# Kernel tuning notes

Measured on AMD Instinct MI355X. Metric: run time of the kernel, lower is better.

The kernel has to match this reference:

```python
import jax, jax.numpy as jnp
import numpy as np

B, N, D, H, CD = 2, 2048, 1024, 16, 3
HD = D // H


def setup_inputs() -> dict:
    key = jax.random.key(0)
    ks = jax.random.split(key, 6)
    x = jax.random.normal(ks[0], (B, N, D), dtype=jnp.float32)
    coords = jax.random.normal(ks[1], (B, N, CD), dtype=jnp.float32)
    attn_bias = jax.random.normal(ks[2], (N, N), dtype=jnp.float32) * 0.1
    Wqkv = jax.random.normal(ks[3], (D, 3 * D), dtype=jnp.float32) * (1.0 / np.sqrt(D))
    bqkv = jnp.zeros((3 * D,), dtype=jnp.float32)
    rel_weight = jax.random.normal(ks[4], (H, CD), dtype=jnp.float32) * 0.02
    return {"x": x, "coords": coords, "attn_bias": attn_bias, "Wqkv": Wqkv,
            "bqkv": bqkv, "rel_weight": rel_weight}


def reference(x, coords, attn_bias, Wqkv, bqkv, rel_weight):
    b, n, d = x.shape
    h, hd = H, HD
    qkv = x @ Wqkv + bqkv                       # (B,N,3D)
    q, k, v = jnp.split(qkv, 3, axis=-1)
    # reshape_for_mha: (B,N,D) -> (B,H,N,hd)
    def heads(t):
        return t.reshape(b, n, h, hd).transpose(0, 2, 1, 3)
    qh, kh, vh = heads(q), heads(k), heads(v)
    # coord_proj[b,h,n] = coords[b,n,:] @ rel_weight[h,:]
    coord_proj = jnp.einsum('bnc,hc->bhn', coords.astype(jnp.float32), rel_weight)
    # flex_attention: scale by 1/sqrt(head_dim) BEFORE score_mod
    scores = jnp.einsum('bhqd,bhkd->bhqk', qh, kh) / np.sqrt(hd)
    scores = scores + coord_proj[:, :, :, None] - coord_proj[:, :, None, :]
    scores = scores + attn_bias[None, None, :, :]   # '2d' additive mask bias
    attn = jax.nn.softmax(scores, axis=-1)
    yh = jnp.einsum('bhqk,bhkd->bhqd', attn, vh)    # (B,H,N,hd)
    return yh.transpose(0, 2, 1, 3).reshape(b, n, d)
```

## Files before the change

### kernel.cpp

```cpp
#include <hip/hip_runtime.h>
#include <hip/hip_bf16.h>
#include <math.h>

typedef __hip_bfloat16 bf16;
typedef __bf16  bf16x8 __attribute__((ext_vector_type(8)));
typedef float   f32x4  __attribute__((ext_vector_type(4)));

#define BB 2
#define NN 2048
#define DD 1024
#define HH 16
#define HD 64
#define LOG2E   1.44269504f
#define SCALE_Q 0.18033688f

__device__ __forceinline__ void glds16(const bf16* g, bf16* l) {
    __builtin_amdgcn_global_load_lds((const __attribute__((address_space(1))) void*)g,
                                     (__attribute__((address_space(3))) void*)l, 16, 0, 0);
}
__device__ __forceinline__ unsigned short bfu(float x) {
    bf16 b = __float2bfloat16(x);
    return __builtin_bit_cast(unsigned short, b);
}

__global__ __launch_bounds__(256) void prep(const float* __restrict__ x,
                                            const float* __restrict__ bias,
                                            const float* __restrict__ W,
                                            const float* __restrict__ coords,
                                            const float* __restrict__ relw,
                                            bf16* __restrict__ xb,
                                            unsigned* __restrict__ pbh,
                                            bf16* __restrict__ Wt,
                                            bf16* __restrict__ cpn) {
    __shared__ bf16 tsm[64][65];
    const int bid = blockIdx.x, tid = threadIdx.x;
    if (bid < 2048) {
        size_t i = ((size_t)bid * 256 + tid) * 8;
        float4 a = *(const float4*)(x + i);
        float4 b = *(const float4*)(x + i + 4);
        bf16 t[8];
        t[0] = __float2bfloat16(a.x); t[1] = __float2bfloat16(a.y);
        t[2] = __float2bfloat16(a.z); t[3] = __float2bfloat16(a.w);
        t[4] = __float2bfloat16(b.x); t[5] = __float2bfloat16(b.y);
        t[6] = __float2bfloat16(b.z); t[7] = __float2bfloat16(b.w);
        *(int4*)(xb + i) = *(int4*)t;
    } else if (bid < 3072) {
        int tt   = (bid - 2048) * 256 + tid;
        int lane = tt & 63;
        int wave = (tt >> 6) & 7;
        int kt   = (tt >> 9) & 31;
        int Qb   = tt >> 14;
        int quad = lane >> 4, l15 = lane & 15;
        unsigned pk[8];
#pragma unroll
        for (int m = 0; m < 8; ++m) {
            int g = m >> 1, rp = m & 1;
            int q = Qb * 128 + wave * 16 + quad * 4 + rp * 2;
            int k = kt * 64 + g * 16 + l15;
            float v0 = LOG2E * bias[(size_t)q * NN + k];
            float v1 = LOG2E * bias[(size_t)(q + 1) * NN + k];
            pk[m] = (unsigned)bfu(v0) | ((unsigned)bfu(v1) << 16);
        }
        int4* dst = (int4*)(pbh + (size_t)tt * 8);
        dst[0] = ((int4*)pk)[0];
        dst[1] = ((int4*)pk)[1];
    } else if (bid < 3840) {
        int idx = bid - 3072;
        int n0 = (idx % 48) * 64;
        int k0 = (idx / 48) * 64;
        int tx = tid & 63, tg = tid >> 6;
#pragma unroll
        for (int i = 0; i < 16; ++i) {
            int r = tg + i * 4;
            tsm[r][tx] = __float2bfloat16(W[(size_t)(k0 + r) * 3072 + n0 + tx]);
        }
        __syncthreads();
#pragma unroll
        for (int i = 0; i < 16; ++i) {
            int r = tg + i * 4;
            Wt[(size_t)(n0 + r) * 1024 + k0 + tx] = tsm[tx][r];
        }
    } else {
        int idx = (bid - 3840) * 256 + tid;
        int n  = idx & (NN - 1);
        int bh = idx >> 11;
        int h  = bh & (HH - 1);
        int b  = bh >> 4;
        float acc = 0.f;
#pragma unroll
        for (int c = 0; c < 3; ++c)
            acc += coords[(size_t)(b * NN + n) * 3 + c] * relw[h * 3 + c];
        cpn[idx] = __float2bfloat16(-LOG2E * acc);
    }
}

__global__ __launch_bounds__(256) void qkv_gemm(const bf16* __restrict__ X,
                                                const bf16* __restrict__ W,
                                                const float* __restrict__ bq,
                                                bf16* __restrict__ qo,
                                                bf16* __restrict__ ko,
                                                bf16* __restrict__ vt) {
    __shared__ __align__(16) bf16 As[128 * 32];
    __shared__ __align__(16) bf16 Bs[128 * 32];
    const int tid  = threadIdx.x;
    const int gid  = blockIdx.x + blockIdx.y * 24;
    const int xcd  = gid & 7;
    const int idx  = gid >> 3;
    const int n0   = (idx >> 2) * 128;
    const int m0   = (xcd * 4 + (idx & 3)) * 128;
    const int wave = tid >> 6, lane = tid & 63, l15 = lane & 15, quad = lane >> 4;
    const int wm   = wave >> 1, wn = wave & 1;

    f32x4 acc[4][4];
    const f32x4 z4 = {0.f, 0.f, 0.f, 0.f};
#pragma unroll
    for (int i = 0; i < 4; ++i)
#pragma unroll
        for (int j = 0; j < 4; ++j) acc[i][j] = z4;

    for (int kt = 0; kt < 1024; kt += 32) {
        __syncthreads();
#pragma unroll
        for (int j = 0; j < 2; ++j) {
            int s   = (wave * 2 + j) * 64 + lane;
            int row = s >> 2;
            int c   = (s & 3) ^ ((row >> 1) & 3);
            glds16(X + (size_t)(m0 + row) * 1024 + kt + c * 8, As + (wave * 2 + j) * 512);
            glds16(W + (size_t)(n0 + row) * 1024 + kt + c * 8, Bs + (wave * 2 + j) * 512);
        }
        __syncthreads();

        bf16x8 a[4], b[4];
#pragma unroll
        for (int mt = 0; mt < 4; ++mt) {
            int ra = wm * 64 + mt * 16 + l15;
            a[mt] = *(const bf16x8*)&As[ra * 32 + ((quad ^ ((ra >> 1) & 3)) * 8)];
        }
#pragma unroll
        for (int nt = 0; nt < 4; ++nt) {
            int rb = wn * 64 + nt * 16 + l15;
            b[nt] = *(const bf16x8*)&Bs[rb * 32 + ((quad ^ ((rb >> 1) & 3)) * 8)];
        }
#pragma unroll
        for (int mt = 0; mt < 4; ++mt)
#pragma unroll
            for (int nt = 0; nt < 4; ++nt)
                acc[mt][nt] = __builtin_amdgcn_mfma_f32_16x16x32_bf16(a[mt], b[nt], acc[mt][nt], 0, 0, 0);
    }

#pragma unroll
    for (int nt = 0; nt < 4; ++nt) {
        int c    = n0 + wn * 64 + nt * 16 + l15;
        int tsel = c >> 10;
        int rem  = c & 1023;
        int h    = rem >> 6, d = rem & 63;
        float bias = bq[c];
        float qs   = (tsel == 0) ? SCALE_Q : 1.0f;
#pragma unroll
        for (int mt = 0; mt < 4; ++mt)
#pragma unroll
            for (int r = 0; r < 4; ++r) {
                int m = m0 + wm * 64 + mt * 16 + quad * 4 + r;
                int b = m >> 11, n = m & (NN - 1);
                bf16 val = __float2bfloat16((acc[mt][nt][r] + bias) * qs);
                if (tsel == 2)
                    vt[((size_t)(b * HH + h) * HD + d) * NN + n] = val;
                else
                    ((tsel == 1) ? ko : qo)[((size_t)(b * HH + h) * NN + n) * HD + d] = val;
            }
    }
}

__global__ __launch_bounds__(512, 4) void attn(const bf16* __restrict__ Q,
                                               const bf16* __restrict__ K,
                                               const bf16* __restrict__ Vt_g,
                                               const bf16* __restrict__ cpn_g,
                                               const unsigned* __restrict__ pbh,
                                               float* __restrict__ out) {
    __shared__ __align__(16) bf16 Ks[2][64 * 64];
    __shared__ __align__(16) bf16 Vs[2][64 * 64];
    __shared__ __align__(16) unsigned PsW[8][16 * 36];
    __shared__ __align__(16) bf16 cpl[NN];
    const int tid  = threadIdx.x;
    const int Qb   = blockIdx.x;
    const int bh   = blockIdx.y;
    const int b    = bh >> 4, h = bh & 15;
    const int q0   = Qb * 128;
    const int wave = tid >> 6, lane = tid & 63, l15 = lane & 15, quad = lane >> 4;
    const size_t base = (size_t)bh * NN * HD;

    if (wave < 4)
        glds16(cpn_g + bh * NN + (wave * 64 + lane) * 8, cpl + wave * 512);

    const int qrow = q0 + wave * 16 + l15;
    bf16x8 qf0 = *(const bf16x8*)&Q[base + (size_t)qrow * HD + quad * 8];
    bf16x8 qf1 = *(const bf16x8*)&Q[base + (size_t)qrow * HD + 32 + quad * 8];

    const int ps   = wave * 64 + lane;
    const int prow = ps >> 3;
    const int pcol = (ps & 7) ^ (prow & 7);

    glds16(K    + base + (size_t)prow * HD + pcol * 8, Ks[0] + wave * 512);
    glds16(Vt_g + base + (size_t)prow * NN + pcol * 8, Vs[0] + wave * 512);

    const unsigned* bptr = pbh + ((((size_t)Qb * 32) * 8 + wave) * 64 + lane) * 8;
    unsigned bvA[8], bvB[8];
    *(int4*)&bvA[0] = ((const int4*)bptr)[0];
    *(int4*)&bvA[4] = ((const int4*)bptr)[1];

    const f32x4 z4 = {0.f, 0.f, 0.f, 0.f};
    f32x4 l4 = z4;
    f32x4 o[4];
#pragma unroll
    for (int t = 0; t < 4; ++t) o[t] = z4;

#define ATTN_TILE(T, CUR, BVC, BVN)                                               \
    {                                                                             \
        __syncthreads();     \
        if ((T) < 31) {                   \
            int kk1 = ((T) + 1) * 64;                                             \
            glds16(K    + base + (size_t)(kk1 + prow) * HD + pcol * 8,            \
                   Ks[(CUR) ^ 1] + wave * 512);                                   \
            glds16(Vt_g + base + (size_t)prow * NN + kk1 + pcol * 8,              \
                   Vs[(CUR) ^ 1] + wave * 512);                                   \
            const unsigned* bp = bptr + (size_t)((T) + 1) * 4096;                 \
            *(int4*)&BVN[0] = ((const int4*)bp)[0];                               \
            *(int4*)&BVN[4] = ((const int4*)bp)[1];                               \
        }                                                                         \
               \
        f32x4 p4[4];                                                              \
        _Pragma("unroll")                                                         \
        for (int g = 0; g < 4; ++g) {                                             \
            float mgv = __bfloat162float(cpl[(T) * 64 + g * 16 + l15]);           \
            unsigned ba = BVC[g * 2], bb2 = BVC[g * 2 + 1];                       \
            f32x4 c0;                                                             \
            c0[0] = __builtin_bit_cast(float, ba << 16) + mgv;                    \
            c0[1] = __builtin_bit_cast(float, ba & 0xffff0000u) + mgv;            \
            c0[2] = __builtin_bit_cast(float, bb2 << 16) + mgv;                   \
            c0[3] = __builtin_bit_cast(float, bb2 & 0xffff0000u) + mgv;           \
            int krow = g * 16 + l15, sw = krow & 7;                               \
            bf16x8 k0 = *(const bf16x8*)&Ks[(CUR)][krow * 64 + ((quad ^ sw) * 8)];         \
            bf16x8 k1 = *(const bf16x8*)&Ks[(CUR)][krow * 64 + (((4 + quad) ^ sw) * 8)];   \
            f32x4 s4 = __builtin_amdgcn_mfma_f32_16x16x32_bf16(qf0, k0, c0, 0, 0, 0);      \
            s4 = __builtin_amdgcn_mfma_f32_16x16x32_bf16(qf1, k1, s4, 0, 0, 0);   \
            f32x4 e;                                                              \
            e[0] = __builtin_amdgcn_exp2f(s4[0]);                                 \
            e[1] = __builtin_amdgcn_exp2f(s4[1]);                                 \
            e[2] = __builtin_amdgcn_exp2f(s4[2]);                                 \
            e[3] = __builtin_amdgcn_exp2f(s4[3]);                                 \
            p4[g] = e;                                                            \
            l4 = l4 + e;                                                          \
        }                                                                         \
                  \
        _Pragma("unroll")                                                         \
        for (int g2 = 0; g2 < 2; ++g2)                                            \
            _Pragma("unroll")                                                     \
            for (int r = 0; r < 4; ++r) {                                         \
                unsigned pk = (unsigned)bfu(p4[g2][r]) |                          \
                              ((unsigned)bfu(p4[g2 + 2][r]) << 16);               \
                PsW[wave][(quad * 4 + r) * 36 + g2 * 16 + l15] = pk;              \
            }                                                                     \
        asm volatile("s_waitcnt lgkmcnt(0)" ::: "memory");                        \
        const int4* pr = (const int4*)&PsW[wave][l15 * 36 + quad * 8];            \
        int4 da = pr[0], db = pr[1];                                              \
        union { unsigned u[4]; bf16x8 v; } u0, u1;                                \
        u0.u[0] = __builtin_amdgcn_perm(da.y, da.x, 0x05040100u);                 \
        u0.u[1] = __builtin_amdgcn_perm(da.w, da.z, 0x05040100u);                 \
        u0.u[2] = __builtin_amdgcn_perm(db.y, db.x, 0x05040100u);                 \
        u0.u[3] = __builtin_amdgcn_perm(db.w, db.z, 0x05040100u);                 \
        u1.u[0] = __builtin_amdgcn_perm(da.y, da.x, 0x07060302u);                 \
        u1.u[1] = __builtin_amdgcn_perm(da.w, da.z, 0x07060302u);                 \
        u1.u[2] = __builtin_amdgcn_perm(db.y, db.x, 0x07060302u);                 \
        u1.u[3] = __builtin_amdgcn_perm(db.w, db.z, 0x07060302u);                 \
                                              \
        __builtin_amdgcn_s_setprio(1);                                            \
        _Pragma("unroll")                                                         \
        for (int tt = 0; tt < 4; ++tt) {                                          \
            int drow = tt * 16 + l15, sw2 = drow & 7;                             \
            bf16x8 v0 = *(const bf16x8*)&Vs[(CUR)][drow * 64 + ((quad ^ sw2) * 8)];        \
            bf16x8 v1 = *(const bf16x8*)&Vs[(CUR)][drow * 64 + (((4 + quad) ^ sw2) * 8)];  \
            o[tt] = __builtin_amdgcn_mfma_f32_16x16x32_bf16(u0.v, v0, o[tt], 0, 0, 0);     \
            o[tt] = __builtin_amdgcn_mfma_f32_16x16x32_bf16(u1.v, v1, o[tt], 0, 0, 0);     \
        }                                                                         \
        __builtin_amdgcn_s_setprio(0);                                            \
    }

    for (int t = 0; t < 32; t += 2) {
        ATTN_TILE(t,     0, bvA, bvB)
        ATTN_TILE(t + 1, 1, bvB, bvA)
    }
#undef ATTN_TILE

    float l_loc[4] = {l4[0], l4[1], l4[2], l4[3]};
#pragma unroll
    for (int r = 0; r < 4; ++r) {
#pragma unroll
        for (int d = 1; d < 16; d <<= 1)
            l_loc[r] += __shfl_xor(l_loc[r], d, 64);
        float inv = 1.0f / l_loc[r];
        int qq = q0 + wave * 16 + quad * 4 + r;
#pragma unroll
        for (int tt = 0; tt < 4; ++tt)
            out[((size_t)(b * NN + qq)) * DD + h * HD + tt * 16 + l15] =
                o[tt][r] * inv;
    }
}

extern "C" void kernel_launch(void* const* d_in, const int* in_sizes, int n_in,
                              void* d_out, int out_size, void* d_ws, size_t ws_size,
                              hipStream_t stream) {
    const float* x      = (const float*)d_in[0];
    const float* coords = (const float*)d_in[1];
    const float* abias  = (const float*)d_in[2];
    const float* Wqkv   = (const float*)d_in[3];
    const float* bqkv   = (const float*)d_in[4];
    const float* relw   = (const float*)d_in[5];
    float* out = (float*)d_out;

    char* ws = (char*)d_ws;
    bf16*     xb  = (bf16*)(ws);
    bf16*     qw  = (bf16*)(ws + 8388608);
    bf16*     kw  = (bf16*)(ws + 16777216);
    bf16*     vt  = (bf16*)(ws + 25165824);
    bf16*     Wt  = (bf16*)(ws + 33554432);
    unsigned* pbh = (unsigned*)(ws + 39845888);
    bf16*     cpb = (bf16*)(ws + 56623104);

    prep    <<<dim3(4096),   256, 0, stream>>>(x, abias, Wqkv, coords, relw,
                                               xb, pbh, Wt, cpb);
    qkv_gemm<<<dim3(24, 32), 256, 0, stream>>>(xb, Wt, bqkv, qw, kw, vt);
    attn    <<<dim3(16, 32), 512, 0, stream>>>(qw, kw, vt, cpb, pbh, out);
}
```

Before: 191.3 us.

## Compute transposed S^T so P stays in registers, removing LDS round-trip

Swaps the MFMA operand order so the QK^T product yields S transposed, with keys permuted through a new K swizzle and a matching bias-prepack layout. The exponentiated probabilities then already sit in the B-operand layout for the PV MFMA, which removes the per-tile LDS write, waitcnt, readback and perm shuffles. The row-sum reduction shrinks to two shuffles and the output store becomes a vectorized float4 write. The cost is a more intricate swizzle and index mapping that must stay consistent across the prep kernel and the attention kernel.

```diff
diff --git a/kernel.cpp b/kernel.cpp
--- a/kernel.cpp
+++ b/kernel.cpp
@@ -51,15 +51,15 @@
         int kt   = (tt >> 9) & 31;
         int Qb   = tt >> 14;
         int quad = lane >> 4, l15 = lane & 15;
+        int q    = Qb * 128 + wave * 16 + l15;
+        const float* brow = bias + (size_t)q * NN + kt * 64 + quad * 8;
         unsigned pk[8];
 #pragma unroll
-        for (int m = 0; m < 8; ++m) {
-            int g = m >> 1, rp = m & 1;
-            int q = Qb * 128 + wave * 16 + quad * 4 + rp * 2;
-            int k = kt * 64 + g * 16 + l15;
-            float v0 = LOG2E * bias[(size_t)q * NN + k];
-            float v1 = LOG2E * bias[(size_t)(q + 1) * NN + k];
-            pk[m] = (unsigned)bfu(v0) | ((unsigned)bfu(v1) << 16);
+        for (int g = 0; g < 4; ++g) {
+            int off = (g >> 1) * 32 + (g & 1) * 4;
+            const float4 bv = *(const float4*)(brow + off);
+            pk[g * 2]     = (unsigned)bfu(LOG2E * bv.x) | ((unsigned)bfu(LOG2E * bv.y) << 16);
+            pk[g * 2 + 1] = (unsigned)bfu(LOG2E * bv.z) | ((unsigned)bfu(LOG2E * bv.w) << 16);
         }
         int4* dst = (int4*)(pbh + (size_t)tt * 8);
         dst[0] = ((int4*)pk)[0];
@@ -179,7 +179,6 @@
                                                float* __restrict__ out) {
     __shared__ __align__(16) bf16 Ks[2][64 * 64];
     __shared__ __align__(16) bf16 Vs[2][64 * 64];
-    __shared__ __align__(16) unsigned PsW[8][16 * 36];
     __shared__ __align__(16) bf16 cpl[NN];
     const int tid  = threadIdx.x;
     const int Qb   = blockIdx.x;
@@ -196,20 +195,26 @@
     bf16x8 qf0 = *(const bf16x8*)&Q[base + (size_t)qrow * HD + quad * 8];
     bf16x8 qf1 = *(const bf16x8*)&Q[base + (size_t)qrow * HD + 32 + quad * 8];
 
-    const int ps   = wave * 64 + lane;
-    const int prow = ps >> 3;
-    const int pcol = (ps & 7) ^ (prow & 7);
-
-    glds16(K    + base + (size_t)prow * HD + pcol * 8, Ks[0] + wave * 512);
-    glds16(Vt_g + base + (size_t)prow * NN + pcol * 8, Vs[0] + wave * 512);
+    const int ps    = wave * 64 + lane;
+    const int prow  = ps >> 3;
+    const int pcolV = (ps & 7) ^ (prow & 7);
+    const int pcolK = (ps & 7) ^ (((prow >> 3) & 3) | ((prow & 1) << 2));
+
+    glds16(K    + base + (size_t)prow * HD + pcolK * 8, Ks[0] + wave * 512);
+    glds16(Vt_g + base + (size_t)prow * NN + pcolV * 8, Vs[0] + wave * 512);
 
     const unsigned* bptr = pbh + ((((size_t)Qb * 32) * 8 + wave) * 64 + lane) * 8;
     unsigned bvA[8], bvB[8];
     *(int4*)&bvA[0] = ((const int4*)bptr)[0];
     *(int4*)&bvA[4] = ((const int4*)bptr)[1];
 
+    const int lrow = ((l15 >> 2) << 3) + (l15 & 3);
+    const int fK   = (l15 >> 2) | ((l15 & 1) << 2);
+    const int ck0  = (quad ^ fK) * 8;
+    const int ck1  = ((4 + quad) ^ fK) * 8;
+
     const f32x4 z4 = {0.f, 0.f, 0.f, 0.f};
-    f32x4 l4 = z4;
+    float l_acc = 0.f;
     f32x4 o[4];
 #pragma unroll
     for (int t = 0; t < 4; ++t) o[t] = z4;
@@ -219,68 +224,58 @@
         __syncthreads();     \
         if ((T) < 31) {                   \
             int kk1 = ((T) + 1) * 64;                                             \
-            glds16(K    + base + (size_t)(kk1 + prow) * HD + pcol * 8,            \
+            glds16(K    + base + (size_t)(kk1 + prow) * HD + pcolK * 8,           \
                    Ks[(CUR) ^ 1] + wave * 512);                                   \
-            glds16(Vt_g + base + (size_t)prow * NN + kk1 + pcol * 8,              \
+            glds16(Vt_g + base + (size_t)prow * NN + kk1 + pcolV * 8,             \
                    Vs[(CUR) ^ 1] + wave * 512);                                   \
             const unsigned* bp = bptr + (size_t)((T) + 1) * 4096;                 \
             *(int4*)&BVN[0] = ((const int4*)bp)[0];                               \
             *(int4*)&BVN[4] = ((const int4*)bp)[1];                               \
         }                                                                         \
-               \
-        f32x4 p4[4];                                                              \
+          \
+          \
+        unsigned w32[8];                                                          \
         _Pragma("unroll")                                                         \
         for (int g = 0; g < 4; ++g) {                                             \
-            float mgv = __bfloat162float(cpl[(T) * 64 + g * 16 + l15]);           \
+            const int kb = (g >> 1) * 32 + (g & 1) * 4;                           \
+            ushort4 mgu = *(const ushort4*)&cpl[(T) * 64 + kb + quad * 8];        \
             unsigned ba = BVC[g * 2], bb2 = BVC[g * 2 + 1];                       \
             f32x4 c0;                                                             \
-            c0[0] = __builtin_bit_cast(float, ba << 16) + mgv;                    \
-            c0[1] = __builtin_bit_cast(float, ba & 0xffff0000u) + mgv;            \
-            c0[2] = __builtin_bit_cast(float, bb2 << 16) + mgv;                   \
-            c0[3] = __builtin_bit_cast(float, bb2 & 0xffff0000u) + mgv;           \
-            int krow = g * 16 + l15, sw = krow & 7;                               \
-            bf16x8 k0 = *(const bf16x8*)&Ks[(CUR)][krow * 64 + ((quad ^ sw) * 8)];         \
-            bf16x8 k1 = *(const bf16x8*)&Ks[(CUR)][krow * 64 + (((4 + quad) ^ sw) * 8)];   \
-            f32x4 s4 = __builtin_amdgcn_mfma_f32_16x16x32_bf16(qf0, k0, c0, 0, 0, 0);      \
-            s4 = __builtin_amdgcn_mfma_f32_16x16x32_bf16(qf1, k1, s4, 0, 0, 0);   \
+            c0[0] = __builtin_bit_cast(float, ba << 16)                           \
+                  + __builtin_bit_cast(float, (unsigned)mgu.x << 16);             \
+            c0[1] = __builtin_bit_cast(float, ba & 0xffff0000u)                   \
+                  + __builtin_bit_cast(float, (unsigned)mgu.y << 16);             \
+            c0[2] = __builtin_bit_cast(float, bb2 << 16)                          \
+                  + __builtin_bit_cast(float, (unsigned)mgu.z << 16);             \
+            c0[3] = __builtin_bit_cast(float, bb2 & 0xffff0000u)                  \
+                  + __builtin_bit_cast(float, (unsigned)mgu.w << 16);             \
+            int krow = kb + lrow;                                                 \
+            bf16x8 k0 = *(const bf16x8*)&Ks[(CUR)][krow * 64 + ck0];              \
+            bf16x8 k1 = *(const bf16x8*)&Ks[(CUR)][krow * 64 + ck1];              \
+            f32x4 s4 = __builtin_amdgcn_mfma_f32_16x16x32_bf16(k0, qf0, c0, 0, 0, 0);      \
+            s4 = __builtin_amdgcn_mfma_f32_16x16x32_bf16(k1, qf1, s4, 0, 0, 0);   \
             f32x4 e;                                                              \
             e[0] = __builtin_amdgcn_exp2f(s4[0]);                                 \
             e[1] = __builtin_amdgcn_exp2f(s4[1]);                                 \
             e[2] = __builtin_amdgcn_exp2f(s4[2]);                                 \
             e[3] = __builtin_amdgcn_exp2f(s4[3]);                                 \
-            p4[g] = e;                                                            \
-            l4 = l4 + e;                                                          \
+            l_acc += (e[0] + e[1]) + (e[2] + e[3]);                               \
+            w32[g * 2]     = (unsigned)bfu(e[0]) | ((unsigned)bfu(e[1]) << 16);   \
+            w32[g * 2 + 1] = (unsigned)bfu(e[2]) | ((unsigned)bfu(e[3]) << 16);   \
         }                                                                         \
                   \
-        _Pragma("unroll")                                                         \
-        for (int g2 = 0; g2 < 2; ++g2)                                            \
-            _Pragma("unroll")                                                     \
-            for (int r = 0; r < 4; ++r) {                                         \
-                unsigned pk = (unsigned)bfu(p4[g2][r]) |                          \
-                              ((unsigned)bfu(p4[g2 + 2][r]) << 16);               \
-                PsW[wave][(quad * 4 + r) * 36 + g2 * 16 + l15] = pk;              \
-            }                                                                     \
-        asm volatile("s_waitcnt lgkmcnt(0)" ::: "memory");                        \
-        const int4* pr = (const int4*)&PsW[wave][l15 * 36 + quad * 8];            \
-        int4 da = pr[0], db = pr[1];                                              \
-        union { unsigned u[4]; bf16x8 v; } u0, u1;                                \
-        u0.u[0] = __builtin_amdgcn_perm(da.y, da.x, 0x05040100u);                 \
-        u0.u[1] = __builtin_amdgcn_perm(da.w, da.z, 0x05040100u);                 \
-        u0.u[2] = __builtin_amdgcn_perm(db.y, db.x, 0x05040100u);                 \
-        u0.u[3] = __builtin_amdgcn_perm(db.w, db.z, 0x05040100u);                 \
-        u1.u[0] = __builtin_amdgcn_perm(da.y, da.x, 0x07060302u);                 \
-        u1.u[1] = __builtin_amdgcn_perm(da.w, da.z, 0x07060302u);                 \
-        u1.u[2] = __builtin_amdgcn_perm(db.y, db.x, 0x07060302u);                 \
-        u1.u[3] = __builtin_amdgcn_perm(db.w, db.z, 0x07060302u);                 \
-                                              \
+        union { unsigned u[4]; bf16x8 v; } B0, B1;                                \
+        B0.u[0] = w32[0]; B0.u[1] = w32[1]; B0.u[2] = w32[2]; B0.u[3] = w32[3];   \
+        B1.u[0] = w32[4]; B1.u[1] = w32[5]; B1.u[2] = w32[6]; B1.u[3] = w32[7];   \
+                                         \
         __builtin_amdgcn_s_setprio(1);                                            \
         _Pragma("unroll")                                                         \
         for (int tt = 0; tt < 4; ++tt) {                                          \
             int drow = tt * 16 + l15, sw2 = drow & 7;                             \
             bf16x8 v0 = *(const bf16x8*)&Vs[(CUR)][drow * 64 + ((quad ^ sw2) * 8)];        \
             bf16x8 v1 = *(const bf16x8*)&Vs[(CUR)][drow * 64 + (((4 + quad) ^ sw2) * 8)];  \
-            o[tt] = __builtin_amdgcn_mfma_f32_16x16x32_bf16(u0.v, v0, o[tt], 0, 0, 0);     \
-            o[tt] = __builtin_amdgcn_mfma_f32_16x16x32_bf16(u1.v, v1, o[tt], 0, 0, 0);     \
+            o[tt] = __builtin_amdgcn_mfma_f32_16x16x32_bf16(v0, B0.v, o[tt], 0, 0, 0);     \
+            o[tt] = __builtin_amdgcn_mfma_f32_16x16x32_bf16(v1, B1.v, o[tt], 0, 0, 0);     \
         }                                                                         \
         __builtin_amdgcn_s_setprio(0);                                            \
     }
@@ -291,18 +286,17 @@
     }
 #undef ATTN_TILE
 
-    float l_loc[4] = {l4[0], l4[1], l4[2], l4[3]};
-#pragma unroll
-    for (int r = 0; r < 4; ++r) {
-#pragma unroll
-        for (int d = 1; d < 16; d <<= 1)
-            l_loc[r] += __shfl_xor(l_loc[r], d, 64);
-        float inv = 1.0f / l_loc[r];
-        int qq = q0 + wave * 16 + quad * 4 + r;
-#pragma unroll
-        for (int tt = 0; tt < 4; ++tt)
-            out[((size_t)(b * NN + qq)) * DD + h * HD + tt * 16 + l15] =
-                o[tt][r] * inv;
+    l_acc += __shfl_xor(l_acc, 16, 64);
+    l_acc += __shfl_xor(l_acc, 32, 64);
+    const float inv = 1.0f / l_acc;
+
+    const int qq = q0 + wave * 16 + l15;
+#pragma unroll
+    for (int tt = 0; tt < 4; ++tt) {
+        f32x4 ov;
+        ov[0] = o[tt][0] * inv; ov[1] = o[tt][1] * inv;
+        ov[2] = o[tt][2] * inv; ov[3] = o[tt][3] * inv;
+        *(f32x4*)&out[((size_t)(b * NN + qq)) * DD + h * HD + tt * 16 + quad * 4] = ov;
     }
 }
 
```

Measured after the change: 193.6 us. Within noise of the previous version (+1.2%).
